# Kernel tuning notes

Measured on AMD Instinct MI355X. Metric: run time of the kernel, lower is better.

Reference implementation:

```python
import jax, jax.numpy as jnp
import numpy as np

EPS = 1e-6  # nn.PairwiseDistance default eps (added to the difference)


def setup_inputs() -> dict:
    key = jax.random.key(0)
    feature = jax.random.normal(key, (16384, 256), dtype=jnp.float32)
    return {"feature": feature}


def reference(feature) -> jnp.ndarray:
    n = feature.shape[0]
    # all-pairs inner products [n, n]
    dots = jnp.matmul(feature, feature.T)
    # mask self-similarity on the diagonal with -1 (as in the torch code)
    dots = dots.at[jnp.diag_indices(n)].set(-1.0)
    # row-wise nearest neighbor (argmax of inner product)
    I = jnp.argmax(dots, axis=1)  # [n] int
    # PairwiseDistance(p=2): ||x1 - x2 + eps||_2
    diff = feature - feature[I] + EPS  # [n, d]
    distances = jnp.sqrt(jnp.sum(diff * diff, axis=1))  # [n]
    loss_uniform = -jnp.mean(jnp.log(n * distances))
    return loss_uniform
```

## Files before the change

kernel.cpp:

```cpp
#include <hip/hip_runtime.h>
#include <hip/hip_bf16.h>
#include <math.h>


#define NROWS 16384
#define DIM   256
#define EPSF  1e-6f

typedef __attribute__((ext_vector_type(4))) float f32x4;

typedef const __attribute__((address_space(1))) void* gas1_t;
typedef __attribute__((address_space(3))) void* las3_t;

__device__ __forceinline__ void glds16(const void* g, void* l) {
    __builtin_amdgcn_global_load_lds((gas1_t)g, (las3_t)l, 16, 0, 0);
}

__device__ __forceinline__ unsigned umax2(unsigned a, unsigned b) {
    return a > b ? a : b;
}

__device__ __forceinline__ unsigned f2e4m3(float f) {
    union { float f; unsigned u; } x; x.f = f;
    const unsigned s = (x.u >> 24) & 0x80u;
    const unsigned au = x.u & 0x7FFFFFFFu;
    const float af = __uint_as_float(au);
    if (au < 0x3C800000u) {
        const int q = (int)(af * 512.0f + 0.5f);
        return s | (unsigned)q;
    }
    const unsigned add = 0x7FFFFu + ((au >> 20) & 1u);
    const unsigned v = au + add;
    const unsigned e = (v >> 23) - 120u;
    return s | (e << 3) | ((v >> 20) & 7u);
}

__global__ __launch_bounds__(256)
void convert_kernel(const float* __restrict__ F, unsigned char* __restrict__ F8,
                    unsigned long long* __restrict__ packed)
{
    const int t = blockIdx.x * 256 + threadIdx.x;
    const float4 a = *reinterpret_cast<const float4*>(F + (size_t)t * 8);
    const float4 b = *reinterpret_cast<const float4*>(F + (size_t)t * 8 + 4);
    const unsigned lo = f2e4m3(a.x) | (f2e4m3(a.y) << 8) |
                        (f2e4m3(a.z) << 16) | (f2e4m3(a.w) << 24);
    const unsigned hi = f2e4m3(b.x) | (f2e4m3(b.y) << 8) |
                        (f2e4m3(b.z) << 16) | (f2e4m3(b.w) << 24);
    uint2 v; v.x = lo; v.y = hi;
    *reinterpret_cast<uint2*>(F8 + (size_t)t * 8) = v;
    if (t < NROWS) packed[t] = 0ull;
}

__global__ __launch_bounds__(256, 3)
void mfma_sym_fp8_kernel(const unsigned char* __restrict__ F8,
                         unsigned long long* __restrict__ packed)
{
    __shared__ __align__(16) unsigned char As[32768];
    __shared__ __align__(16) unsigned char Bs[2 * 8192];

    const int tid  = threadIdx.x;
    const int w    = tid >> 6;
    const int l    = tid & 63;
    const int rs   = (int)blockIdx.x >> 3;
    const int ck   = (int)blockIdx.x & 7;
    const int span = 128 - rs;
    const int t0   = rs + ((span * ck) >> 3);
    const int t1   = rs + ((span * (ck + 1)) >> 3);
    if (t0 >= t1) return;

    const int row0 = rs * 128;
    const int wrow = (w >> 1) * 64;
    const int wcol = (w & 1) * 64;
    const int lc   = l & 15;
    const int lr4  = l >> 4;
    const int k16r = lr4 >> 1;
    const int odd  = lr4 & 1;

    #pragma unroll
    for (int m = 0; m < 8; ++m) {
        const int q = 8 * w + m;
        glds16(F8 + (size_t)(row0 + (q & 1) * 64 + l) * DIM + (q >> 1) * 16,
               &As[q * 1024]);
    }

    #pragma unroll
    for (int q2 = 0; q2 < 2; ++q2) {
        const int col = q2 * 64 + l;
        glds16(F8 + (size_t)(t0 * 128 + col) * DIM + w * 16,
               &Bs[(2 * w + q2) * 1024]);
    }

    const long* __restrict__ Al = reinterpret_cast<const long*>(As);

    f32x4 acc[4][4];
    #pragma unroll
    for (int i = 0; i < 4; ++i)
        #pragma unroll
        for (int j = 0; j < 4; ++j)
            acc[i][j] = (f32x4){512.f, 512.f, 512.f, 512.f};

    unsigned best[4][4] = {};

    for (int t = t0; t < t1; ++t) {
        const bool dt = (t == rs);
        #pragma unroll
        for (int ss = 0; ss < 4; ++ss) {
            __syncthreads();

            const int nt  = (ss < 3) ? t : t + 1;
            const int nss = (ss < 3) ? ss + 1 : 0;
            if (nt < t1) {
                #pragma unroll
                for (int q2 = 0; q2 < 2; ++q2) {
                    const int col = q2 * 64 + l;
                    glds16(F8 + (size_t)(nt * 128 + col) * DIM + nss * 64 + w * 16,
                           &Bs[((ss & 1) ^ 1) * 8192 + (2 * w + q2) * 1024]);
                }
            }

            const long* __restrict__ Bl =
                reinterpret_cast<const long*>(Bs) + (ss & 1) * 1024;

            #pragma unroll
            for (int h = 0; h < 2; ++h) {
                const int kk = h * 2 + k16r;
                long afv[4], bfv[4];
                #pragma unroll
                for (int i = 0; i < 4; ++i)
                    afv[i] = Al[(ss * 4 + kk) * 256 + (wrow + i * 16 + lc) * 2 + odd];
                #pragma unroll
                for (int j = 0; j < 4; ++j)
                    bfv[j] = Bl[kk * 256 + (wcol + j * 16 + lc) * 2 + odd];
                #pragma unroll
                for (int j = 0; j < 4; ++j)
                    #pragma unroll
                    for (int i = 0; i < 4; ++i)
                        acc[i][j] = __builtin_amdgcn_mfma_f32_16x16x32_fp8_fp8(
                            afv[i], bfv[j], acc[i][j], 0, 0, 0);
            }
        }

        const int tl = t - t0;
        unsigned cbA[4];
        #pragma unroll
        for (int j = 0; j < 4; ++j)
            cbA[j] = 2047u - (unsigned)(tl * 128 + wcol + j * 16 + lc);

        #pragma unroll
        for (int j = 0; j < 4; ++j) {
            unsigned kb = 0u;
            #pragma unroll
            for (int i = 0; i < 4; ++i)
                #pragma unroll
                for (int g = 0; g < 4; ++g) {
                    const int r_loc = wrow + i * 16 + lr4 * 4 + g;
                    unsigned m = __float_as_uint(acc[i][j][g]) & 0xFFFFF800u;
                    if (dt && (wcol + j * 16 + lc == r_loc)) m = 0u;
                    best[i][g] = umax2(best[i][g], m | cbA[j]);
                    kb = umax2(kb, m | (unsigned)(127 - r_loc));
                    acc[i][j][g] = 512.f;
                }
            kb = umax2(kb, (unsigned)__shfl_xor((int)kb, 16));
            kb = umax2(kb, (unsigned)__shfl_xor((int)kb, 32));
            if (lr4 == 0) {
                const unsigned grow = (unsigned)row0 + (127u - (kb & 0x7FFu));
                atomicMax(&packed[t * 128 + wcol + j * 16 + lc],
                          ((unsigned long long)(kb & 0xFFFFF800u) << 32) |
                          (0xFFFFFFFFu - grow));
            }
        }
    }

    #pragma unroll
    for (int i = 0; i < 4; ++i)
        #pragma unroll
        for (int g = 0; g < 4; ++g) {
            unsigned key = best[i][g];
            #pragma unroll
            for (int m = 8; m >= 1; m >>= 1)
                key = umax2(key, (unsigned)__shfl_xor((int)key, m));
            if (lc == 0) {
                const int r = row0 + wrow + i * 16 + lr4 * 4 + g;
                const unsigned c = (unsigned)(t0 * 128) + (2047u - (key & 0x7FFu));
                atomicMax(&packed[r],
                          ((unsigned long long)(key & 0xFFFFF800u) << 32) |
                          (0xFFFFFFFFu - c));
            }
        }
}

__global__ __launch_bounds__(256)
void dist_loss_kernel(const float* __restrict__ F,
                      const unsigned long long* __restrict__ packed,
                      double* __restrict__ partials)
{
    const int tid  = threadIdx.x;
    const int lane = tid & 63;
    const int w    = tid >> 6;
    const int gw   = blockIdx.x * 4 + w;
    double local = 0.0;
    for (int r = gw; r < NROWS; r += 1024) {
        const unsigned long long p = packed[r];
        const int idx = (int)(0xFFFFFFFFu - (unsigned)(p & 0xFFFFFFFFull));
        const float4 a = *reinterpret_cast<const float4*>(
            F + (size_t)r * DIM + (lane << 2));
        const float4 b = *reinterpret_cast<const float4*>(
            F + (size_t)idx * DIM + (lane << 2));
        const float dx = a.x - b.x + EPSF;
        const float dy = a.y - b.y + EPSF;
        const float dz = a.z - b.z + EPSF;
        const float dw = a.w - b.w + EPSF;
        float ss = dx * dx + dy * dy + dz * dz + dw * dw;
        #pragma unroll
        for (int m = 32; m >= 1; m >>= 1) ss += __shfl_xor(ss, m);
        if (lane == 0)
            local += 0.5 * log((double)ss) + log((double)NROWS);
    }
    __shared__ double sm[4];
    if (lane == 0) sm[w] = local;
    __syncthreads();
    if (tid == 0) partials[blockIdx.x] = sm[0] + sm[1] + sm[2] + sm[3];
}

__global__ __launch_bounds__(256)
void finalize_kernel(const double* __restrict__ partials, float* __restrict__ out)
{
    const int tid = threadIdx.x;
    double v = partials[tid];
    #pragma unroll
    for (int m = 32; m >= 1; m >>= 1) v += __shfl_xor(v, m);
    __shared__ double sm[4];
    if ((tid & 63) == 0) sm[tid >> 6] = v;
    __syncthreads();
    if (tid == 0) out[0] = (float)(-(sm[0] + sm[1] + sm[2] + sm[3]) / (double)NROWS);
}

extern "C" void kernel_launch(void* const* d_in, const int* in_sizes, int n_in,
                              void* d_out, int out_size, void* d_ws, size_t ws_size,
                              hipStream_t stream)
{
    const float* F   = (const float*)d_in[0];
    float*       out = (float*)d_out;

    char* ws = (char*)d_ws;
    unsigned char*      F8       = (unsigned char*)ws;
    unsigned long long* packed   = (unsigned long long*)(ws + 4194304);
    double*             partials = (double*)(ws + 4325376);

    convert_kernel<<<2048, 256, 0, stream>>>(F, F8, packed);
    mfma_sym_fp8_kernel<<<1024, 256, 0, stream>>>(F8, packed);
    dist_loss_kernel<<<256, 256, 0, stream>>>(F, packed, partials);
    finalize_kernel<<<1, 256, 0, stream>>>(partials, out);
}
```

Measured before the change: 119.8 us.

## Replace column atomicMax with per-tile scratch writes reduced in loss kernel

New measurement: 150.3 us. +25.4%, slower.

```diff
diff --git a/kernel.cpp b/kernel.cpp
--- a/kernel.cpp
+++ b/kernel.cpp
@@ -17,6 +17,11 @@
 }
 
 __device__ __forceinline__ unsigned umax2(unsigned a, unsigned b) {
+    return a > b ? a : b;
+}
+
+__device__ __forceinline__ unsigned long long umax64(unsigned long long a,
+                                                     unsigned long long b) {
     return a > b ? a : b;
 }
 
@@ -53,10 +58,12 @@
 
 __global__ __launch_bounds__(256, 3)
 void mfma_sym_fp8_kernel(const unsigned char* __restrict__ F8,
-                         unsigned long long* __restrict__ packed)
+                         unsigned long long* __restrict__ packed,
+                         unsigned long long* __restrict__ scratch)
 {
     __shared__ __align__(16) unsigned char As[32768];
     __shared__ __align__(16) unsigned char Bs[2 * 8192];
+    __shared__ unsigned cmb[256];
 
     const int tid  = threadIdx.x;
     const int w    = tid >> 6;
@@ -106,6 +113,15 @@
         #pragma unroll
         for (int ss = 0; ss < 4; ++ss) {
             __syncthreads();
+
+            if (ss == 0 && t > t0 && w < 2) {
+                const int c = w * 64 + l;
+                const unsigned km = umax2(cmb[c], cmb[128 + c]);
+                const unsigned grow = (unsigned)row0 + (127u - (km & 0x7FFu));
+                scratch[((size_t)(t - 1) * 128 + rs) * 128 + c] =
+                    ((unsigned long long)(km & 0xFFFFF800u) << 32) |
+                    (0xFFFFFFFFu - grow);
+            }
 
             const int nt  = (ss < 3) ? t : t + 1;
             const int nss = (ss < 3) ? ss + 1 : 0;
@@ -162,13 +178,18 @@
                 }
             kb = umax2(kb, (unsigned)__shfl_xor((int)kb, 16));
             kb = umax2(kb, (unsigned)__shfl_xor((int)kb, 32));
-            if (lr4 == 0) {
-                const unsigned grow = (unsigned)row0 + (127u - (kb & 0x7FFu));
-                atomicMax(&packed[t * 128 + wcol + j * 16 + lc],
-                          ((unsigned long long)(kb & 0xFFFFF800u) << 32) |
-                          (0xFFFFFFFFu - grow));
-            }
+            if (lr4 == 0) cmb[(w >> 1) * 128 + wcol + j * 16 + lc] = kb;
         }
+    }
+
+    __syncthreads();
+    if (w < 2) {
+        const int c = w * 64 + l;
+        const unsigned km = umax2(cmb[c], cmb[128 + c]);
+        const unsigned grow = (unsigned)row0 + (127u - (km & 0x7FFu));
+        scratch[((size_t)(t1 - 1) * 128 + rs) * 128 + c] =
+            ((unsigned long long)(km & 0xFFFFF800u) << 32) |
+            (0xFFFFFFFFu - grow);
     }
 
     #pragma unroll
@@ -192,16 +213,34 @@
 __global__ __launch_bounds__(256)
 void dist_loss_kernel(const float* __restrict__ F,
                       const unsigned long long* __restrict__ packed,
+                      const unsigned long long* __restrict__ scratch,
                       double* __restrict__ partials)
 {
-    const int tid  = threadIdx.x;
+    __shared__ unsigned long long sm[128];
+    __shared__ double sd[4];
+
+    const int t   = blockIdx.x;
+    const int tid = threadIdx.x;
+    const int c   = tid & 127;
+    const int h   = tid >> 7;
+
+    unsigned long long m = 0ull;
+    const unsigned long long* base = scratch + (size_t)t * 16384;
+    for (int rsd = h; rsd <= t; rsd += 2)
+        m = umax64(m, base[rsd * 128 + c]);
+    if (h == 0) sm[c] = m;
+    __syncthreads();
+    if (h == 1) sm[c] = umax64(sm[c], m);
+    __syncthreads();
+
+    const int w    = tid >> 6;
     const int lane = tid & 63;
-    const int w    = tid >> 6;
-    const int gw   = blockIdx.x * 4 + w;
     double local = 0.0;
-    for (int r = gw; r < NROWS; r += 1024) {
-        const unsigned long long p = packed[r];
-        const int idx = (int)(0xFFFFFFFFu - (unsigned)(p & 0xFFFFFFFFull));
+    for (int rr = w; rr < 128; rr += 4) {
+        const int r = t * 128 + rr;
+        const unsigned long long best = umax64(packed[r], sm[rr]);
+        const int idx = (int)(0xFFFFFFFFu - (unsigned)(best & 0xFFFFFFFFull));
+
         const float4 a = *reinterpret_cast<const float4*>(
             F + (size_t)r * DIM + (lane << 2));
         const float4 b = *reinterpret_cast<const float4*>(
@@ -212,27 +251,26 @@
         const float dw = a.w - b.w + EPSF;
         float ss = dx * dx + dy * dy + dz * dz + dw * dw;
         #pragma unroll
-        for (int m = 32; m >= 1; m >>= 1) ss += __shfl_xor(ss, m);
+        for (int mm = 32; mm >= 1; mm >>= 1) ss += __shfl_xor(ss, mm);
         if (lane == 0)
             local += 0.5 * log((double)ss) + log((double)NROWS);
     }
-    __shared__ double sm[4];
-    if (lane == 0) sm[w] = local;
-    __syncthreads();
-    if (tid == 0) partials[blockIdx.x] = sm[0] + sm[1] + sm[2] + sm[3];
-}
-
-__global__ __launch_bounds__(256)
+    if (lane == 0) sd[w] = local;
+    __syncthreads();
+    if (tid == 0) partials[t] = sd[0] + sd[1] + sd[2] + sd[3];
+}
+
+__global__ __launch_bounds__(128)
 void finalize_kernel(const double* __restrict__ partials, float* __restrict__ out)
 {
     const int tid = threadIdx.x;
     double v = partials[tid];
     #pragma unroll
     for (int m = 32; m >= 1; m >>= 1) v += __shfl_xor(v, m);
-    __shared__ double sm[4];
-    if ((tid & 63) == 0) sm[tid >> 6] = v;
-    __syncthreads();
-    if (tid == 0) out[0] = (float)(-(sm[0] + sm[1] + sm[2] + sm[3]) / (double)NROWS);
+    __shared__ double sd[2];
+    if ((tid & 63) == 0) sd[tid >> 6] = v;
+    __syncthreads();
+    if (tid == 0) out[0] = (float)(-(sd[0] + sd[1]) / (double)NROWS);
 }
 
 extern "C" void kernel_launch(void* const* d_in, const int* in_sizes, int n_in,
@@ -245,10 +283,11 @@
     char* ws = (char*)d_ws;
     unsigned char*      F8       = (unsigned char*)ws;
     unsigned long long* packed   = (unsigned long long*)(ws + 4194304);
-    double*             partials = (double*)(ws + 4325376);
+    unsigned long long* scratch  = (unsigned long long*)(ws + 4325376);
+    double*             partials = (double*)(ws + 21102592);
 
     convert_kernel<<<2048, 256, 0, stream>>>(F, F8, packed);
-    mfma_sym_fp8_kernel<<<1024, 256, 0, stream>>>(F8, packed);
-    dist_loss_kernel<<<256, 256, 0, stream>>>(F, packed, partials);
-    finalize_kernel<<<1, 256, 0, stream>>>(partials, out);
-}
+    mfma_sym_fp8_kernel<<<1024, 256, 0, stream>>>(F8, packed, scratch);
+    dist_loss_kernel<<<128, 256, 0, stream>>>(F, packed, scratch, partials);
+    finalize_kernel<<<1, 128, 0, stream>>>(partials, out);
+}
```
